# Kernel tuning notes

Hardware: AMD Instinct MI355X
Metric: run time of the kernel (lower is better)

Reference implementation:

```python
import jax, jax.numpy as jnp
import numpy as np

D_MODEL = 1024
NUM_HEADS = 16
HEAD_DIM = D_MODEL // NUM_HEADS


def setup_inputs() -> dict:
    key = jax.random.key(0)
    k1, k2, k3 = jax.random.split(key, 3)
    x = jax.random.normal(k1, (2, 2048, D_MODEL), dtype=jnp.float32)
    # trunc_normal init approximated by clipped normal with same std
    std_qkv = np.sqrt(2.0 / (D_MODEL + 3 * D_MODEL)).astype(np.float32)
    std_o = np.sqrt(2.0 / (D_MODEL + D_MODEL)).astype(np.float32)
    w_qkv = jnp.clip(jax.random.normal(k2, (3 * D_MODEL, D_MODEL), dtype=jnp.float32) * std_qkv,
                     -3 * std_qkv, 3 * std_qkv)
    w_o = jnp.clip(jax.random.normal(k3, (D_MODEL, D_MODEL), dtype=jnp.float32) * std_o,
                   -3 * std_o, 3 * std_o)
    return {"x": x, "w_qkv": w_qkv, "w_o": w_o}


def reference(x, w_qkv, w_o):
    b, s, d = x.shape
    h, hd = NUM_HEADS, HEAD_DIM
    # QKV projection: weight is [d_out, d_in]
    qkv = jnp.einsum('od,bsd->bso', w_qkv, x)  # [b, s, 3d]
    q, k, v = jnp.split(qkv, 3, axis=-1)
    # [b, s, d] -> [b, h, s, hd]
    def to_heads(t):
        return t.reshape(b, s, h, hd).transpose(0, 2, 1, 3)
    q_mh, k_mh, v_mh = to_heads(q), to_heads(k), to_heads(v)
    scale = 1.0 / jnp.sqrt(jnp.asarray(hd, dtype=x.dtype))
    scores = jnp.einsum('bhmd,bhnd->bhmn', q_mh, k_mh) * scale  # [b,h,s,s]
    causal = jnp.tril(jnp.ones((s, s), dtype=bool))
    scores = jnp.where(causal, scores, -jnp.inf)
    attn = jax.nn.softmax(scores, axis=-1)
    out = jnp.einsum('bhmn,bhnd->bhmd', attn, v_mh)  # [b,h,s,hd]
    out = out.transpose(0, 2, 1, 3).reshape(b, s, d)
    return jnp.einsum('od,bsd->bso', w_o, out)
```

## Files before the change

### kernel.cpp

```cpp
#include <hip/hip_runtime.h>

constexpr int SEQ = 2048;
constexpr int DM = 1024;
constexpr int NH = 16;
constexpr int BATCH = 2;
constexpr int MTOT = BATCH * SEQ;

typedef __bf16 bf16x8 __attribute__((ext_vector_type(8)));
typedef __bf16 bf16x4 __attribute__((ext_vector_type(4)));
typedef float f32x4 __attribute__((ext_vector_type(4)));

#define MFMA16(a, b, c) __builtin_amdgcn_mfma_f32_16x16x32_bf16((a), (b), (c), 0, 0, 0)

__device__ __forceinline__ void async_copy16(const void* g, void* l) {
  __builtin_amdgcn_global_load_lds((const __attribute__((address_space(1))) void*)g,
                                   (__attribute__((address_space(3))) void*)l, 16, 0, 0);
}

__device__ __forceinline__ void xcd_swizzle(int& bx, int& by) {
  const int gx = gridDim.x;
  const int nwg = gx * gridDim.y;
  const int bid = blockIdx.y * gx + blockIdx.x;
  const int cpx = nwg >> 3;
  const int v = (bid & 7) * cpx + (bid >> 3);
  by = v / gx;
  bx = v - by * gx;
}

__global__ void sentinel_fill(float* out, int n) {
  int i = blockIdx.x * blockDim.x + threadIdx.x;
  for (; i < n; i += gridDim.x * blockDim.x) out[i] = 0.25f;
}

__global__ __launch_bounds__(256) void cvt_all(const float* __restrict__ x,
                                               const float* __restrict__ wq,
                                               const float* __restrict__ wo,
                                               __bf16* __restrict__ xb,
                                               __bf16* __restrict__ wqb,
                                               __bf16* __restrict__ wob) {
  const long i = (long)(blockIdx.x * 256 + threadIdx.x) * 8;
  const float* src;
  __bf16* dst;
  long off;
  if (i < 4194304) { src = x; dst = xb; off = i; }
  else if (i < 7340032) { src = wq; dst = wqb; off = i - 4194304; }
  else { src = wo; dst = wob; off = i - 7340032; }
  f32x4 lo = *(const f32x4*)(src + off);
  f32x4 hi = *(const f32x4*)(src + off + 4);
  bf16x8 r;
#pragma unroll
  for (int j = 0; j < 4; ++j) { r[j] = (__bf16)lo[j]; r[4 + j] = (__bf16)hi[j]; }
  *(bf16x8*)(dst + off) = r;
}

template <typename OutT>
__global__ __launch_bounds__(256) void gemm_bt(const __bf16* __restrict__ A,
                                               const __bf16* __restrict__ B,
                                               OutT* __restrict__ C,
                                               int M, int N, int K, int lda,
                                               float nanSig) {
  __shared__ alignas(16) __bf16 As[3][128 * 32];
  __shared__ alignas(16) __bf16 Bs[3][128 * 32];
  const int tid = threadIdx.x;
  const int lane = tid & 63;
  const int wave = tid >> 6;
  const int lr = lane & 15;
  const int quad = lane >> 4;
  const int wm = (wave >> 1) * 64;
  const int wn = (wave & 1) * 64;
  int bx, by;
  xcd_swizzle(bx, by);
  const int m0 = by * 128;
  const int n0 = bx * 128;

  const int ra = tid >> 2;
  const int ca = (tid & 3) * 8;
  const __bf16* gA0 = A + (long)(m0 + ra) * lda + ca;
  const __bf16* gA1 = A + (long)(m0 + 64 + ra) * lda + ca;
  const __bf16* gB0 = B + (long)(n0 + ra) * K + ca;
  const __bf16* gB1 = B + (long)(n0 + 64 + ra) * K + ca;

  f32x4 acc[4][4];
#pragma unroll
  for (int i = 0; i < 4; ++i)
#pragma unroll
    for (int j = 0; j < 4; ++j) acc[i][j] = (f32x4){0.f, 0.f, 0.f, 0.f};

  auto stage = [&](int bi, int k0) {
    async_copy16(gA0 + k0, &As[bi][wave * 512]);
    async_copy16(gA1 + k0, &As[bi][2048 + wave * 512]);
    async_copy16(gB0 + k0, &Bs[bi][wave * 512]);
    async_copy16(gB1 + k0, &Bs[bi][2048 + wave * 512]);
  };

  const int nt = K >> 5;
  stage(0, 0);
  if (nt > 1) stage(1, 32);

  int cur = 0;
  for (int t = 0; t < nt; ++t) {
    if (t + 1 < nt) {
      asm volatile("s_waitcnt vmcnt(4)" ::: "memory");
    } else {
      asm volatile("s_waitcnt vmcnt(0)" ::: "memory");
    }
    __builtin_amdgcn_sched_barrier(0);
    __builtin_amdgcn_s_barrier();
    if (t + 2 < nt) stage(cur == 0 ? 2 : cur - 1, (t + 2) * 32);

    bf16x8 af[4], bfr[4];
#pragma unroll
    for (int i = 0; i < 4; ++i)
      af[i] = *(const bf16x8*)&As[cur][(wm + i * 16 + lr) * 32 + quad * 8];
#pragma unroll
    for (int j = 0; j < 4; ++j)
      bfr[j] = *(const bf16x8*)&Bs[cur][(wn + j * 16 + lr) * 32 + quad * 8];
    __builtin_amdgcn_s_setprio(1);
#pragma unroll
    for (int i = 0; i < 4; ++i)
#pragma unroll
      for (int j = 0; j < 4; ++j) acc[i][j] = MFMA16(af[i], bfr[j], acc[i][j]);
    __builtin_amdgcn_s_setprio(0);
    cur = (cur == 2) ? 0 : cur + 1;
  }

#pragma unroll
  for (int i = 0; i < 4; ++i) {
    const int row = m0 + wm + i * 16 + quad * 4;
#pragma unroll
    for (int j = 0; j < 4; ++j) {
      const int col = n0 + wn + j * 16 + lr;
#pragma unroll
      for (int r = 0; r < 4; ++r) {
        float v = acc[i][j][r];
        if (!(v == v)) v = nanSig;
        C[(long)(row + r) * N + col] = (OutT)v;
      }
    }
  }
}

template <typename OutT>
__global__ __launch_bounds__(256) void gemm_bt64(const __bf16* __restrict__ A,
                                                 const __bf16* __restrict__ B,
                                                 OutT* __restrict__ C,
                                                 int M, int N, int K, int lda,
                                                 float nanSig) {
  __shared__ alignas(16) __bf16 As[3][64 * 32];
  __shared__ alignas(16) __bf16 Bs[3][128 * 32];
  const int tid = threadIdx.x;
  const int lane = tid & 63;
  const int wave = tid >> 6;
  const int lr = lane & 15;
  const int quad = lane >> 4;
  const int wm = (wave >> 1) * 32;
  const int wn = (wave & 1) * 64;
  int bx, by;
  xcd_swizzle(bx, by);
  const int m0 = by * 64;
  const int n0 = bx * 128;

  const int ra = tid >> 2;
  const int ca = (tid & 3) * 8;
  const __bf16* gA0 = A + (long)(m0 + ra) * lda + ca;
  const __bf16* gB0 = B + (long)(n0 + ra) * K + ca;
  const __bf16* gB1 = B + (long)(n0 + 64 + ra) * K + ca;

  f32x4 acc[2][4];
#pragma unroll
  for (int i = 0; i < 2; ++i)
#pragma unroll
    for (int j = 0; j < 4; ++j) acc[i][j] = (f32x4){0.f, 0.f, 0.f, 0.f};

  auto stage = [&](int bi, int k0) {
    async_copy16(gA0 + k0, &As[bi][wave * 512]);
    async_copy16(gB0 + k0, &Bs[bi][wave * 512]);
    async_copy16(gB1 + k0, &Bs[bi][2048 + wave * 512]);
  };

  const int nt = K >> 5;
  stage(0, 0);
  if (nt > 1) stage(1, 32);

  int cur = 0;
  for (int t = 0; t < nt; ++t) {
    if (t + 1 < nt) {
      asm volatile("s_waitcnt vmcnt(3)" ::: "memory");
    } else {
      asm volatile("s_waitcnt vmcnt(0)" ::: "memory");
    }
    __builtin_amdgcn_sched_barrier(0);
    __builtin_amdgcn_s_barrier();
    if (t + 2 < nt) stage(cur == 0 ? 2 : cur - 1, (t + 2) * 32);

    bf16x8 af[2], bfr[4];
#pragma unroll
    for (int i = 0; i < 2; ++i)
      af[i] = *(const bf16x8*)&As[cur][(wm + i * 16 + lr) * 32 + quad * 8];
#pragma unroll
    for (int j = 0; j < 4; ++j)
      bfr[j] = *(const bf16x8*)&Bs[cur][(wn + j * 16 + lr) * 32 + quad * 8];
    __builtin_amdgcn_s_setprio(1);
#pragma unroll
    for (int i = 0; i < 2; ++i)
#pragma unroll
      for (int j = 0; j < 4; ++j) acc[i][j] = MFMA16(af[i], bfr[j], acc[i][j]);
    __builtin_amdgcn_s_setprio(0);
    cur = (cur == 2) ? 0 : cur + 1;
  }

#pragma unroll
  for (int i = 0; i < 2; ++i) {
    const int row = m0 + wm + i * 16 + quad * 4;
#pragma unroll
    for (int j = 0; j < 4; ++j) {
      const int col = n0 + wn + j * 16 + lr;
#pragma unroll
      for (int r = 0; r < 4; ++r) {
        float v = acc[i][j][r];
        if (!(v == v)) v = nanSig;
        C[(long)(row + r) * N + col] = (OutT)v;
      }
    }
  }
}

template <int F32>
__device__ __forceinline__ bf16x8 load_cvt8(const void* base, long off) {
  if constexpr (F32) {
    const float* p = (const float*)base + off;
    f32x4 lo = *(const f32x4*)p;
    f32x4 hi = *(const f32x4*)(p + 4);
    bf16x8 r;
#pragma unroll
    for (int j = 0; j < 4; ++j) { r[j] = (__bf16)lo[j]; r[4 + j] = (__bf16)hi[j]; }
    return r;
  } else {
    return *(const bf16x8*)((const __bf16*)base + off);
  }
}

template <int AF32, int BF32, typename OutT>
__global__ __launch_bounds__(256) void gemm_nt(const void* __restrict__ Av,
                                               const void* __restrict__ Bv,
                                               OutT* __restrict__ C,
                                               int M, int N, int K, int lda,
                                               float nanSig) {
  __shared__ alignas(16) __bf16 As[128 * 32];
  __shared__ alignas(16) __bf16 Bs[128 * 32];
  const int tid = threadIdx.x;
  const int lane = tid & 63;
  const int wave = tid >> 6;
  const int lr = lane & 15;
  const int quad = lane >> 4;
  const int wm = (wave >> 1) * 64;
  const int wn = (wave & 1) * 64;
  const int m0 = blockIdx.y * 128;
  const int n0 = blockIdx.x * 128;

  const int r0 = tid >> 2;
  const int r1 = 64 + (tid >> 2);
  const int cc = (tid & 3) * 8;
  const long aBase0 = (long)(m0 + r0) * lda + cc;
  const long aBase1 = (long)(m0 + r1) * lda + cc;
  const long bBase0 = (long)(n0 + r0) * K + cc;
  const long bBase1 = (long)(n0 + r1) * K + cc;
  __bf16* lA0 = &As[r0 * 32 + cc];
  __bf16* lA1 = &As[r1 * 32 + cc];
  __bf16* lB0 = &Bs[r0 * 32 + cc];
  __bf16* lB1 = &Bs[r1 * 32 + cc];

  f32x4 acc[4][4];
#pragma unroll
  for (int i = 0; i < 4; ++i)
#pragma unroll
    for (int j = 0; j < 4; ++j) acc[i][j] = (f32x4){0.f, 0.f, 0.f, 0.f};

  for (int k0 = 0; k0 < K; k0 += 32) {
    bf16x8 va0 = load_cvt8<AF32>(Av, aBase0 + k0);
    bf16x8 va1 = load_cvt8<AF32>(Av, aBase1 + k0);
    bf16x8 vb0 = load_cvt8<BF32>(Bv, bBase0 + k0);
    bf16x8 vb1 = load_cvt8<BF32>(Bv, bBase1 + k0);
    __syncthreads();
    *(bf16x8*)lA0 = va0;
    *(bf16x8*)lA1 = va1;
    *(bf16x8*)lB0 = vb0;
    *(bf16x8*)lB1 = vb1;
    __syncthreads();
    bf16x8 af[4], bfr[4];
#pragma unroll
    for (int i = 0; i < 4; ++i) af[i] = *(const bf16x8*)&As[(wm + i * 16 + lr) * 32 + quad * 8];
#pragma unroll
    for (int j = 0; j < 4; ++j) bfr[j] = *(const bf16x8*)&Bs[(wn + j * 16 + lr) * 32 + quad * 8];
#pragma unroll
    for (int i = 0; i < 4; ++i)
#pragma unroll
      for (int j = 0; j < 4; ++j) acc[i][j] = MFMA16(af[i], bfr[j], acc[i][j]);
  }

#pragma unroll
  for (int i = 0; i < 4; ++i) {
    const int row = m0 + wm + i * 16 + quad * 4;
#pragma unroll
    for (int j = 0; j < 4; ++j) {
      const int col = n0 + wn + j * 16 + lr;
#pragma unroll
      for (int r = 0; r < 4; ++r) {
        float v = acc[i][j][r];
        if (!(v == v)) v = nanSig;
        C[(long)(row + r) * N + col] = (OutT)v;
      }
    }
  }
}

__global__ __launch_bounds__(512, 2) void attn_fwd(__bf16* __restrict__ qkv) {
  const int jj = blockIdx.x;
  const int h = blockIdx.y;
  const int b = blockIdx.z;
  const int tid = threadIdx.x;
  const int lane = tid & 63;
  const int wave = tid >> 6;
  const int ps = wave >> 2;
  const int pi = 2 * jj + ps;
  const int q0A = pi * 64;
  const int q0B = (31 - pi) * 64;
  const int lr = lane & 15;
  const int quad = lane >> 4;
  const int wq = (wave & 3) * 16;

  __shared__ alignas(16) __bf16 Ks[2][64 * 72];
  __shared__ alignas(16) __bf16 Vt[2][64 * 72];
  __shared__ alignas(16) __bf16 Pq[256 * 72];

  __bf16* pqw = &Pq[wave * 32 * 72];
  const long base = (long)b * SEQ * 3072;
  const int qi[2] = {q0A + wq + lr, q0B + wq + lr};

  bf16x8 b_q[2][2];
#pragma unroll
  for (int qg = 0; qg < 2; ++qg) {
    const long rowoff = base + (long)qi[qg] * 3072 + h * 64;
    b_q[qg][0] = *(const bf16x8*)(qkv + rowoff + quad * 8);
    b_q[qg][1] = *(const bf16x8*)(qkv + rowoff + 32 + quad * 8);
  }

  const float NEGS = -30000.f;
  const float SC = 0.18033688f;
  float m_i[2] = {NEGS, NEGS}, l_i[2] = {0.f, 0.f};
  f32x4 o_acc[2][4];
#pragma unroll
  for (int qg = 0; qg < 2; ++qg)
#pragma unroll
    for (int dt = 0; dt < 4; ++dt) o_acc[qg][dt] = (f32x4){0.f, 0.f, 0.f, 0.f};

  const int r_ = tid >> 3;
  const int col_ = (tid & 7) * 8;
  const int l8 = tid & 7;
  const int sw = (l8 & 3) << 3;
  const bool oddr = (tid >> 3) & 1;
  const int jb = oddr ? 4 : 0;

  const int Tb = 32 - 2 * jj;
  const int Tp = 32 - pi;

  bf16x8 kreg, vreg;
  auto loadTile = [&](int t) {
    const long ro = base + ((long)t * 64 + r_) * 3072 + h * 64 + col_;
    kreg = *(const bf16x8*)(qkv + ro + 1024);
    vreg = *(const bf16x8*)(qkv + ro + 2048);
  };
  auto stageTile = [&](int bi) {
    __bf16* ks = &Ks[bi][0];
    __bf16* vt = &Vt[bi][0];
    *(bf16x8*)&ks[r_ * 72 + col_] = kreg;
    const int rr = (r_ & ~1) ^ sw;
    int vd[4], od[4];
    __builtin_memcpy(vd, &vreg, 16);
#pragma unroll
    for (int i = 0; i < 4; ++i) od[i] = __shfl_xor(vd[i], 8);
#pragma unroll
    for (int i = 0; i < 4; ++i) {
      const int j = jb + i;
      const int a = vd[j >> 1], bb = od[j >> 1];
      const int lo = oddr ? bb : a;
      const int hi = oddr ? a : bb;
      const int pair = (j & 1) ? (int)(((unsigned)lo >> 16) | (hi & 0xffff0000))
                               : (int)((lo & 0xffff) | (hi << 16));
      *(int*)&vt[(col_ + j) * 72 + rr] = pair;
    }
  };

  loadTile(0);
  stageTile(0);
  loadTile(1);
  __syncthreads();

  for (int t = 0; t < Tb; ++t) {
    const int cur = t & 1;
    const int kv0 = t * 64;
    const bool active = (t < Tp);
    const bool actA = (kv0 <= q0A + wq + 15);

    f32x4 st[2][4];
#pragma unroll
    for (int kt = 0; kt < 4; ++kt) {
      st[1][kt] = (f32x4){0.f, 0.f, 0.f, 0.f};
      st[0][kt] = (f32x4){0.f, 0.f, 0.f, 0.f};
    }
    if (active) {
      __builtin_amdgcn_s_setprio(1);
#pragma unroll
      for (int ks = 0; ks < 2; ++ks) {
        bf16x8 ak[4];
#pragma unroll
        for (int kt = 0; kt < 4; ++kt)
          ak[kt] = *(const bf16x8*)&Ks[cur][(kt * 16 + lr) * 72 + ks * 32 + quad * 8];
#pragma unroll
        for (int kt = 0; kt < 4; ++kt) st[1][kt] = MFMA16(ak[kt], b_q[1][ks], st[1][kt]);
        if (actA) {
#pragma unroll
          for (int kt = 0; kt < 4; ++kt) st[0][kt] = MFMA16(ak[kt], b_q[0][ks], st[0][kt]);
        }
      }
      __builtin_amdgcn_s_setprio(0);
    }

    if (t + 1 < Tb) stageTile(cur ^ 1);
    if (t + 2 < Tb) loadTile(t + 2);

    if (active) {
#pragma unroll
      for (int qg = 1; qg >= 0; --qg) {
        if (qg == 0 && !actA) continue;
        const int q0X = (qg == 0) ? q0A : q0B;
        if (kv0 + 64 <= q0X + wq) {
#pragma unroll
          for (int kt = 0; kt < 4; ++kt)
#pragma unroll
            for (int r = 0; r < 4; ++r) st[qg][kt][r] *= SC;
        } else {
#pragma unroll
          for (int kt = 0; kt < 4; ++kt) {
            const int d0 = kv0 + kt * 16 + quad * 4 - qi[qg];
#pragma unroll
            for (int r = 0; r < 4; ++r)
              st[qg][kt][r] = (d0 + r <= 0) ? st[qg][kt][r] * SC : NEGS;
          }
        }
        float mx = st[qg][0][0];
#pragma unroll
        for (int kt = 0; kt < 4; ++kt)
#pragma unroll
          for (int r = 0; r < 4; ++r) mx = fmaxf(mx, st[qg][kt][r]);
        mx = fmaxf(mx, __shfl_xor(mx, 16));
        mx = fmaxf(mx, __shfl_xor(mx, 32));
        const bool noresc = __all(mx - m_i[qg] <= 8.f);
        const float mnew = noresc ? m_i[qg] : fmaxf(m_i[qg], mx);
        float rs = 0.f;
#pragma unroll
        for (int kt = 0; kt < 4; ++kt)
#pragma unroll
          for (int r = 0; r < 4; ++r) {
            const float p = exp2f(st[qg][kt][r] - mnew);
            st[qg][kt][r] = p;
            rs += p;
          }
        rs += __shfl_xor(rs, 16);
        rs += __shfl_xor(rs, 32);
#pragma unroll
        for (int kt = 0; kt < 4; ++kt) {
          bf16x4 pv;
#pragma unroll
          for (int r = 0; r < 4; ++r) pv[r] = (__bf16)st[qg][kt][r];
          *(bf16x4*)&pqw[(qg * 16 + lr) * 72 + kt * 16 + quad * 4] = pv;
        }
        if (noresc) {
          l_i[qg] += rs;
        } else {
          const float alpha = exp2f(m_i[qg] - mnew);
          l_i[qg] = l_i[qg] * alpha + rs;
          m_i[qg] = mnew;
#pragma unroll
          for (int dt = 0; dt < 4; ++dt)
#pragma unroll
            for (int r = 0; r < 4; ++r) o_acc[qg][dt][r] *= alpha;
        }
      }

      asm volatile("s_waitcnt lgkmcnt(0)" ::: "memory");
      __builtin_amdgcn_sched_barrier(0);

      __builtin_amdgcn_s_setprio(1);
#pragma unroll
      for (int ks = 0; ks < 2; ++ks) {
        bf16x8 av[4];
#pragma unroll
        for (int dt = 0; dt < 4; ++dt) {
          const int blk = ((ks << 2) + quad) ^ ((2 * dt + (lr >> 3)) & 3);
          av[dt] = *(const bf16x8*)&Vt[cur][(dt * 16 + lr) * 72 + (blk << 3)];
        }
        {
          bf16x8 bp = *(const bf16x8*)&pqw[(16 + lr) * 72 + ks * 32 + quad * 8];
#pragma unroll
          for (int dt = 0; dt < 4; ++dt) o_acc[1][dt] = MFMA16(av[dt], bp, o_acc[1][dt]);
        }
        if (actA) {
          bf16x8 bp = *(const bf16x8*)&pqw[lr * 72 + ks * 32 + quad * 8];
#pragma unroll
          for (int dt = 0; dt < 4; ++dt) o_acc[0][dt] = MFMA16(av[dt], bp, o_acc[0][dt]);
        }
      }
      __builtin_amdgcn_s_setprio(0);
    }

    __syncthreads();
  }

#pragma unroll
  for (int qg = 0; qg < 2; ++qg) {
    const float inv = 1.f / fmaxf(l_i[qg], 1e-30f);
    const long obase = base + (long)qi[qg] * 3072 + h * 64 + quad * 4;
#pragma unroll
    for (int dt = 0; dt < 4; ++dt) {
      bf16x4 ov;
#pragma unroll
      for (int r = 0; r < 4; ++r) ov[r] = (__bf16)(o_acc[qg][dt][r] * inv);
      *(bf16x4*)(qkv + obase + dt * 16) = ov;
    }
  }
}

extern "C" void kernel_launch(void* const* d_in, const int* in_sizes, int n_in,
                              void* d_out, int out_size, void* d_ws, size_t ws_size,
                              hipStream_t stream) {
  const float* x = (const float*)d_in[0];
  const float* w_qkv = (const float*)d_in[1];
  const float* w_o = (const float*)d_in[2];
  for (int i = 0; i < n_in; ++i) {
    if (in_sizes[i] == MTOT * DM) x = (const float*)d_in[i];
    else if (in_sizes[i] == 3 * DM * DM) w_qkv = (const float*)d_in[i];
    else if (in_sizes[i] == DM * DM) w_o = (const float*)d_in[i];
  }
  float* out = (float*)d_out;

  const size_t qkvBytes = (size_t)MTOT * 3072 * 2;
  const size_t xbBytes = (size_t)MTOT * DM * 2;
  const size_t wqBytes = (size_t)3 * DM * DM * 2;
  const size_t woBytes = (size_t)DM * DM * 2;
  const size_t needFast = qkvBytes + xbBytes + wqBytes + woBytes;

  __bf16* qkv = (__bf16*)d_ws;

  if (ws_size >= needFast) {
    __bf16* xb = (__bf16*)((char*)d_ws + qkvBytes);
    __bf16* wqb = (__bf16*)((char*)d_ws + qkvBytes + xbBytes);
    __bf16* wob = (__bf16*)((char*)d_ws + qkvBytes + xbBytes + wqBytes);
    cvt_all<<<4096, 256, 0, stream>>>(x, w_qkv, w_o, xb, wqb, wob);
    gemm_bt<__bf16><<<dim3(3072 / 128, MTOT / 128), 256, 0, stream>>>(
        xb, wqb, qkv, MTOT, 3072, DM, DM, 1e4f);
    attn_fwd<<<dim3(8, NH, BATCH), 512, 0, stream>>>(qkv);
    gemm_bt64<float><<<dim3(DM / 128, MTOT / 64), 256, 0, stream>>>(
        qkv, wob, out, MTOT, DM, DM, 3072, 2e4f);
  } else if (ws_size >= qkvBytes) {
    gemm_nt<1, 1, __bf16><<<dim3(3072 / 128, MTOT / 128), 256, 0, stream>>>(
        x, w_qkv, qkv, MTOT, 3072, DM, DM, 1e4f);
    attn_fwd<<<dim3(8, NH, BATCH), 512, 0, stream>>>(qkv);
    gemm_nt<0, 1, float><<<dim3(DM / 128, MTOT / 128), 256, 0, stream>>>(
        qkv, w_o, out, MTOT, DM, DM, 3072, 2e4f);
  } else {
    sentinel_fill<<<256, 256, 0, stream>>>(out, out_size);
  }
}
```

Before: 206.3 us.

## Split attention work so each wave group handles one query block per pair

Each workgroup now takes one mirrored pair of query blocks (pi and 31-pi), with the first four waves on the late block and the last four on the early block, instead of each wave handling both blocks of a pair across two pairs per workgroup. This halves per-wave register state (one Q fragment, one accumulator set, half the P buffer), raises the occupancy hint to 4 workgroups, and doubles the grid to 512 workgroups. The cost is that every workgroup now loads and stages K/V tiles for only 128 query rows instead of 256, doubling K/V traffic per query, and the early-block waves sit idle for most iterations while the late-block waves work.

```diff
diff --git a/kernel.cpp b/kernel.cpp
--- a/kernel.cpp
+++ b/kernel.cpp
@@ -314,45 +314,42 @@
   }
 }
 
-__global__ __launch_bounds__(512, 2) void attn_fwd(__bf16* __restrict__ qkv) {
-  const int jj = blockIdx.x;
+__global__ __launch_bounds__(512, 4) void attn_fwd(__bf16* __restrict__ qkv) {
+  const int pi = blockIdx.x;
   const int h = blockIdx.y;
   const int b = blockIdx.z;
+  const int q0A = pi * 64;
+  const int q0B = (31 - pi) * 64;
   const int tid = threadIdx.x;
   const int lane = tid & 63;
   const int wave = tid >> 6;
-  const int ps = wave >> 2;
-  const int pi = 2 * jj + ps;
-  const int q0A = pi * 64;
-  const int q0B = (31 - pi) * 64;
+  const int grp = wave >> 2;
+  const int q0X = grp ? q0A : q0B;
   const int lr = lane & 15;
   const int quad = lane >> 4;
   const int wq = (wave & 3) * 16;
+  const int qi = q0X + wq + lr;
 
   __shared__ alignas(16) __bf16 Ks[2][64 * 72];
   __shared__ alignas(16) __bf16 Vt[2][64 * 72];
-  __shared__ alignas(16) __bf16 Pq[256 * 72];
-
-  __bf16* pqw = &Pq[wave * 32 * 72];
+  __shared__ alignas(16) __bf16 Pq[128 * 72];
+
+  __bf16* pqw = &Pq[wave * 16 * 72];
   const long base = (long)b * SEQ * 3072;
-  const int qi[2] = {q0A + wq + lr, q0B + wq + lr};
-
-  bf16x8 b_q[2][2];
-#pragma unroll
-  for (int qg = 0; qg < 2; ++qg) {
-    const long rowoff = base + (long)qi[qg] * 3072 + h * 64;
-    b_q[qg][0] = *(const bf16x8*)(qkv + rowoff + quad * 8);
-    b_q[qg][1] = *(const bf16x8*)(qkv + rowoff + 32 + quad * 8);
+
+  bf16x8 b_q[2];
+  {
+    const long rowoff = base + (long)qi * 3072 + h * 64;
+    b_q[0] = *(const bf16x8*)(qkv + rowoff + quad * 8);
+    b_q[1] = *(const bf16x8*)(qkv + rowoff + 32 + quad * 8);
   }
 
   const float NEGS = -30000.f;
   const float SC = 0.18033688f;
-  float m_i[2] = {NEGS, NEGS}, l_i[2] = {0.f, 0.f};
-  f32x4 o_acc[2][4];
-#pragma unroll
-  for (int qg = 0; qg < 2; ++qg)
-#pragma unroll
-    for (int dt = 0; dt < 4; ++dt) o_acc[qg][dt] = (f32x4){0.f, 0.f, 0.f, 0.f};
+  float m_i = NEGS, l_i = 0.f;
+  f32x4 o_acc[4];
+#pragma unroll
+  for (int dt = 0; dt < 4; ++dt) o_acc[dt] = (f32x4){0.f, 0.f, 0.f, 0.f};
 
   const int r_ = tid >> 3;
   const int col_ = (tid & 7) * 8;
@@ -361,8 +358,7 @@
   const bool oddr = (tid >> 3) & 1;
   const int jb = oddr ? 4 : 0;
 
-  const int Tb = 32 - 2 * jj;
-  const int Tp = 32 - pi;
+  const int Tb = 32 - pi;
 
   bf16x8 kreg, vreg;
   auto loadTile = [&](int t) {
@@ -399,16 +395,12 @@
   for (int t = 0; t < Tb; ++t) {
     const int cur = t & 1;
     const int kv0 = t * 64;
-    const bool active = (t < Tp);
-    const bool actA = (kv0 <= q0A + wq + 15);
-
-    f32x4 st[2][4];
-#pragma unroll
-    for (int kt = 0; kt < 4; ++kt) {
-      st[1][kt] = (f32x4){0.f, 0.f, 0.f, 0.f};
-      st[0][kt] = (f32x4){0.f, 0.f, 0.f, 0.f};
-    }
-    if (active) {
+    const bool act = (grp == 0) || (kv0 <= q0A + wq + 15);
+
+    f32x4 st[4];
+#pragma unroll
+    for (int kt = 0; kt < 4; ++kt) st[kt] = (f32x4){0.f, 0.f, 0.f, 0.f};
+    if (act) {
       __builtin_amdgcn_s_setprio(1);
 #pragma unroll
       for (int ks = 0; ks < 2; ++ks) {
@@ -417,11 +409,7 @@
         for (int kt = 0; kt < 4; ++kt)
           ak[kt] = *(const bf16x8*)&Ks[cur][(kt * 16 + lr) * 72 + ks * 32 + quad * 8];
 #pragma unroll
-        for (int kt = 0; kt < 4; ++kt) st[1][kt] = MFMA16(ak[kt], b_q[1][ks], st[1][kt]);
-        if (actA) {
-#pragma unroll
-          for (int kt = 0; kt < 4; ++kt) st[0][kt] = MFMA16(ak[kt], b_q[0][ks], st[0][kt]);
-        }
+        for (int kt = 0; kt < 4; ++kt) st[kt] = MFMA16(ak[kt], b_q[ks], st[kt]);
       }
       __builtin_amdgcn_s_setprio(0);
     }
@@ -429,63 +417,58 @@
     if (t + 1 < Tb) stageTile(cur ^ 1);
     if (t + 2 < Tb) loadTile(t + 2);
 
-    if (active) {
-#pragma unroll
-      for (int qg = 1; qg >= 0; --qg) {
-        if (qg == 0 && !actA) continue;
-        const int q0X = (qg == 0) ? q0A : q0B;
-        if (kv0 + 64 <= q0X + wq) {
-#pragma unroll
-          for (int kt = 0; kt < 4; ++kt)
-#pragma unroll
-            for (int r = 0; r < 4; ++r) st[qg][kt][r] *= SC;
-        } else {
-#pragma unroll
-          for (int kt = 0; kt < 4; ++kt) {
-            const int d0 = kv0 + kt * 16 + quad * 4 - qi[qg];
-#pragma unroll
-            for (int r = 0; r < 4; ++r)
-              st[qg][kt][r] = (d0 + r <= 0) ? st[qg][kt][r] * SC : NEGS;
-          }
+    if (act) {
+      if (kv0 + 64 <= q0X + wq) {
+#pragma unroll
+        for (int kt = 0; kt < 4; ++kt)
+#pragma unroll
+          for (int r = 0; r < 4; ++r) st[kt][r] *= SC;
+      } else {
+#pragma unroll
+        for (int kt = 0; kt < 4; ++kt) {
+          const int d0 = kv0 + kt * 16 + quad * 4 - qi;
+#pragma unroll
+          for (int r = 0; r < 4; ++r)
+            st[kt][r] = (d0 + r <= 0) ? st[kt][r] * SC : NEGS;
         }
-        float mx = st[qg][0][0];
-#pragma unroll
-        for (int kt = 0; kt < 4; ++kt)
-#pragma unroll
-          for (int r = 0; r < 4; ++r) mx = fmaxf(mx, st[qg][kt][r]);
-        mx = fmaxf(mx, __shfl_xor(mx, 16));
-        mx = fmaxf(mx, __shfl_xor(mx, 32));
-        const bool noresc = __all(mx - m_i[qg] <= 8.f);
-        const float mnew = noresc ? m_i[qg] : fmaxf(m_i[qg], mx);
-        float rs = 0.f;
-#pragma unroll
-        for (int kt = 0; kt < 4; ++kt)
-#pragma unroll
-          for (int r = 0; r < 4; ++r) {
-            const float p = exp2f(st[qg][kt][r] - mnew);
-            st[qg][kt][r] = p;
-            rs += p;
-          }
-        rs += __shfl_xor(rs, 16);
-        rs += __shfl_xor(rs, 32);
-#pragma unroll
-        for (int kt = 0; kt < 4; ++kt) {
-          bf16x4 pv;
-#pragma unroll
-          for (int r = 0; r < 4; ++r) pv[r] = (__bf16)st[qg][kt][r];
-          *(bf16x4*)&pqw[(qg * 16 + lr) * 72 + kt * 16 + quad * 4] = pv;
+      }
+      float mx = st[0][0];
+#pragma unroll
+      for (int kt = 0; kt < 4; ++kt)
+#pragma unroll
+        for (int r = 0; r < 4; ++r) mx = fmaxf(mx, st[kt][r]);
+      mx = fmaxf(mx, __shfl_xor(mx, 16));
+      mx = fmaxf(mx, __shfl_xor(mx, 32));
+      const bool noresc = __all(mx - m_i <= 8.f);
+      const float mnew = noresc ? m_i : fmaxf(m_i, mx);
+      float rs = 0.f;
+#pragma unroll
+      for (int kt = 0; kt < 4; ++kt)
+#pragma unroll
+        for (int r = 0; r < 4; ++r) {
+          const float p = exp2f(st[kt][r] - mnew);
+          st[kt][r] = p;
+          rs += p;
         }
-        if (noresc) {
-          l_i[qg] += rs;
-        } else {
-          const float alpha = exp2f(m_i[qg] - mnew);
-          l_i[qg] = l_i[qg] * alpha + rs;
-          m_i[qg] = mnew;
-#pragma unroll
-          for (int dt = 0; dt < 4; ++dt)
-#pragma unroll
-            for (int r = 0; r < 4; ++r) o_acc[qg][dt][r] *= alpha;
-        }
+      rs += __shfl_xor(rs, 16);
+      rs += __shfl_xor(rs, 32);
+#pragma unroll
+      for (int kt = 0; kt < 4; ++kt) {
+        bf16x4 pv;
+#pragma unroll
+        for (int r = 0; r < 4; ++r) pv[r] = (__bf16)st[kt][r];
+        *(bf16x4*)&pqw[lr * 72 + kt * 16 + quad * 4] = pv;
+      }
+      if (noresc) {
+        l_i += rs;
+      } else {
+        const float alpha = exp2f(m_i - mnew);
+        l_i = l_i * alpha + rs;
+        m_i = mnew;
+#pragma unroll
+        for (int dt = 0; dt < 4; ++dt)
+#pragma unroll
+          for (int r = 0; r < 4; ++r) o_acc[dt][r] *= alpha;
       }
 
       asm volatile("s_waitcnt lgkmcnt(0)" ::: "memory");
@@ -500,16 +483,9 @@
           const int blk = ((ks << 2) + quad) ^ ((2 * dt + (lr >> 3)) & 3);
           av[dt] = *(const bf16x8*)&Vt[cur][(dt * 16 + lr) * 72 + (blk << 3)];
         }
-        {
-          bf16x8 bp = *(const bf16x8*)&pqw[(16 + lr) * 72 + ks * 32 + quad * 8];
-#pragma unroll
-          for (int dt = 0; dt < 4; ++dt) o_acc[1][dt] = MFMA16(av[dt], bp, o_acc[1][dt]);
-        }
-        if (actA) {
-          bf16x8 bp = *(const bf16x8*)&pqw[lr * 72 + ks * 32 + quad * 8];
-#pragma unroll
-          for (int dt = 0; dt < 4; ++dt) o_acc[0][dt] = MFMA16(av[dt], bp, o_acc[0][dt]);
-        }
+        bf16x8 bp = *(const bf16x8*)&pqw[lr * 72 + ks * 32 + quad * 8];
+#pragma unroll
+        for (int dt = 0; dt < 4; ++dt) o_acc[dt] = MFMA16(av[dt], bp, o_acc[dt]);
       }
       __builtin_amdgcn_s_setprio(0);
     }
@@ -517,15 +493,14 @@
     __syncthreads();
   }
 
-#pragma unroll
-  for (int qg = 0; qg < 2; ++qg) {
-    const float inv = 1.f / fmaxf(l_i[qg], 1e-30f);
-    const long obase = base + (long)qi[qg] * 3072 + h * 64 + quad * 4;
+  {
+    const float inv = 1.f / fmaxf(l_i, 1e-30f);
+    const long obase = base + (long)qi * 3072 + h * 64 + quad * 4;
 #pragma unroll
     for (int dt = 0; dt < 4; ++dt) {
       bf16x4 ov;
 #pragma unroll
-      for (int r = 0; r < 4; ++r) ov[r] = (__bf16)(o_acc[qg][dt][r] * inv);
+      for (int r = 0; r < 4; ++r) ov[r] = (__bf16)(o_acc[dt][r] * inv);
       *(bf16x4*)(qkv + obase + dt * 16) = ov;
     }
   }
@@ -559,13 +534,13 @@
     cvt_all<<<4096, 256, 0, stream>>>(x, w_qkv, w_o, xb, wqb, wob);
     gemm_bt<__bf16><<<dim3(3072 / 128, MTOT / 128), 256, 0, stream>>>(
         xb, wqb, qkv, MTOT, 3072, DM, DM, 1e4f);
-    attn_fwd<<<dim3(8, NH, BATCH), 512, 0, stream>>>(qkv);
+    attn_fwd<<<dim3(16, NH, BATCH), 512, 0, stream>>>(qkv);
     gemm_bt64<float><<<dim3(DM / 128, MTOT / 64), 256, 0, stream>>>(
         qkv, wob, out, MTOT, DM, DM, 3072, 2e4f);
   } else if (ws_size >= qkvBytes) {
     gemm_nt<1, 1, __bf16><<<dim3(3072 / 128, MTOT / 128), 256, 0, stream>>>(
         x, w_qkv, qkv, MTOT, 3072, DM, DM, 1e4f);
-    attn_fwd<<<dim3(8, NH, BATCH), 512, 0, stream>>>(qkv);
+    attn_fwd<<<dim3(16, NH, BATCH), 512, 0, stream>>>(qkv);
     gemm_nt<0, 1, float><<<dim3(DM / 128, MTOT / 128), 256, 0, stream>>>(
         qkv, w_o, out, MTOT, DM, DM, 3072, 2e4f);
   } else {
```

Result: no change. 209.3 us (median of 2 runs) (+1.4%).
